# Performance work log

Measured on AMD Instinct MI355X. Metric: run time of the kernel, lower is better.

The kernel has to match this reference:

```python
import jax, jax.numpy as jnp
import numpy as np

N_NODES = 100000
N_EDGES = 600000
IN_FEATS = 128
N_HIDDEN = 128
N_CLASSES = 64


def _glorot(key, shape):
    fan_in, fan_out = shape[1], shape[0]
    lim = np.sqrt(6.0 / (fan_in + fan_out)).astype(np.float32)
    return jax.random.uniform(key, shape, jnp.float32, -lim, lim)


def setup_inputs() -> dict:
    key = jax.random.key(0)
    ks = jax.random.split(key, 12)
    x = jax.random.normal(ks[0], (N_NODES, IN_FEATS), jnp.float32)
    edge_src = jax.random.randint(ks[1], (N_EDGES,), 0, N_NODES, jnp.int64 if jax.config.jax_enable_x64 else jnp.int32)
    edge_dst = jax.random.randint(ks[2], (N_EDGES,), 0, N_NODES, jnp.int64 if jax.config.jax_enable_x64 else jnp.int32)
    dims = [(IN_FEATS, N_HIDDEN), (N_HIDDEN, N_HIDDEN), (N_HIDDEN, N_CLASSES)]
    inp = {"x": x, "edge_src": edge_src, "edge_dst": edge_dst}
    for i, (din, dout) in enumerate(dims, start=1):
        inp[f"W_self{i}"] = _glorot(ks[2 + 3 * i], (dout, din))
        inp[f"W_neigh{i}"] = _glorot(ks[3 + 3 * i], (dout, din))
        inp[f"b{i}"] = jnp.zeros((dout,), jnp.float32)
    return inp


def _sage_conv(h, edge_src, edge_dst, W_self, W_neigh, b):
    # mean-aggregate neighbor features: gather at src, segment-mean at dst
    msgs = h[edge_src]                                   # [E, din] irregular gather
    agg = jax.ops.segment_sum(msgs, edge_dst, num_segments=h.shape[0])
    deg = jax.ops.segment_sum(jnp.ones_like(edge_dst, dtype=h.dtype), edge_dst,
                              num_segments=h.shape[0])
    h_neigh = agg / jnp.maximum(deg, 1.0)[:, None]
    # fc_self(h) + fc_neigh(h_neigh) + bias  (DGL SAGEConv 'mean')
    return h @ W_self.T + h_neigh @ W_neigh.T + b


def reference(x, edge_src, edge_dst,
              W_self1, W_neigh1, b1,
              W_self2, W_neigh2, b2,
              W_self3, W_neigh3, b3):
    h = _sage_conv(x, edge_src, edge_dst, W_self1, W_neigh1, b1)
    h = jax.nn.relu(h)  # dropout is identity at inference
    h = _sage_conv(h, edge_src, edge_dst, W_self2, W_neigh2, b2)
    h = jax.nn.relu(h)
    h = _sage_conv(h, edge_src, edge_dst, W_self3, W_neigh3, b3)
    return h
```

## Files before the change

kernel.cpp:

```cpp
#include <hip/hip_runtime.h>

#define NN 100000
#define NE 600000
#define FD 128
#define NB ((NN + 255) / 256)

typedef __attribute__((ext_vector_type(8))) short bf16x8;
typedef __attribute__((ext_vector_type(4))) float f32x4;

__device__ __forceinline__ unsigned short f2bf(float x) {
    unsigned int u = __float_as_uint(x);
    u += 0x7FFFu + ((u >> 16) & 1u);
    return (unsigned short)(u >> 16);
}

__global__ __launch_bounds__(256) void hist_kernel(const int* __restrict__ dst,
                                                   int* __restrict__ cnt, int E) {
    int e = blockIdx.x * 256 + threadIdx.x;
    if (e < E) atomicAdd(&cnt[dst[e]], 1);
}

__global__ __launch_bounds__(256) void scan_blocks(const int* __restrict__ cnt,
                                                   int* __restrict__ bsum) {
    __shared__ int s[256];
    int i = blockIdx.x * 256 + threadIdx.x;
    int t = threadIdx.x;
    s[t] = (i < NN) ? cnt[i] : 0;
    __syncthreads();
    for (int off = 128; off > 0; off >>= 1) {
        if (t < off) s[t] += s[t + off];
        __syncthreads();
    }
    if (t == 0) bsum[blockIdx.x] = s[0];
}

__global__ __launch_bounds__(512) void scan_top(int* __restrict__ bsum,
                                                int* __restrict__ row_ptr) {
    __shared__ int s[512];
    int t = threadIdx.x;
    int v = (t < NB) ? bsum[t] : 0;
    s[t] = v;
    __syncthreads();
    for (int off = 1; off < 512; off <<= 1) {
        int x = (t >= off) ? s[t - off] : 0;
        __syncthreads();
        s[t] += x;
        __syncthreads();
    }
    if (t < NB) bsum[t] = s[t] - v;
    if (t == 0) row_ptr[NN] = NE;
}

__global__ __launch_bounds__(256) void scan_write(const int* __restrict__ cnt,
                                                  const int* __restrict__ bofs,
                                                  int* __restrict__ row_ptr) {
    __shared__ int s[256];
    int i = blockIdx.x * 256 + threadIdx.x;
    int t = threadIdx.x;
    int v = (i < NN) ? cnt[i] : 0;
    s[t] = v;
    __syncthreads();
    for (int off = 1; off < 256; off <<= 1) {
        int x = (t >= off) ? s[t - off] : 0;
        __syncthreads();
        s[t] += x;
        __syncthreads();
    }
    if (i < NN) row_ptr[i] = s[t] - v + bofs[blockIdx.x];
}

__global__ __launch_bounds__(256) void fill_kernel(const int* __restrict__ src,
                                                   const int* __restrict__ dst,
                                                   int* __restrict__ cursor,
                                                   int* __restrict__ col, int E) {
    int e = blockIdx.x * 256 + threadIdx.x;
    if (e < E) {
        int p = atomicAdd(&cursor[dst[e]], 1);
        col[p] = src[e];
    }
}

__global__ __launch_bounds__(256) void cvt_kernel(const float* __restrict__ x,
                                                  unsigned short* __restrict__ xb,
                                                  int n4) {
    int i = blockIdx.x * 256 + threadIdx.x;
    if (i < n4) {
        float4 v = reinterpret_cast<const float4*>(x)[i];
        uint2 o;
        o.x = (unsigned)f2bf(v.x) | ((unsigned)f2bf(v.y) << 16);
        o.y = (unsigned)f2bf(v.z) | ((unsigned)f2bf(v.w) << 16);
        reinterpret_cast<uint2*>(xb)[i] = o;
    }
}

__device__ __forceinline__ void bf2_acc(unsigned v, float& ax, float& ay) {
    ax += __uint_as_float(v << 16);
    ay += __uint_as_float(v & 0xFFFF0000u);
}

__global__ __launch_bounds__(256) void agg_kernel(const unsigned short* __restrict__ h,
                                                  const int* __restrict__ rp,
                                                  const int* __restrict__ col,
                                                  unsigned short* __restrict__ agg) {
    int w    = (blockIdx.x * 256 + threadIdx.x) >> 6;
    int lane = threadIdx.x & 63;
    if (w >= NN) return;
    int beg = __builtin_amdgcn_readfirstlane(rp[w]);
    int end = __builtin_amdgcn_readfirstlane(rp[w + 1]);
    const unsigned short* hl = h + lane * 2;
    float ax = 0.f, ay = 0.f;
    int e = beg;
    for (; e + 4 <= end; e += 4) {
        int s0 = col[e + 0], s1 = col[e + 1], s2 = col[e + 2], s3 = col[e + 3];
        unsigned v0 = *reinterpret_cast<const unsigned*>(hl + (size_t)s0 * FD);
        unsigned v1 = *reinterpret_cast<const unsigned*>(hl + (size_t)s1 * FD);
        unsigned v2 = *reinterpret_cast<const unsigned*>(hl + (size_t)s2 * FD);
        unsigned v3 = *reinterpret_cast<const unsigned*>(hl + (size_t)s3 * FD);
        bf2_acc(v0, ax, ay);
        bf2_acc(v1, ax, ay);
        bf2_acc(v2, ax, ay);
        bf2_acc(v3, ax, ay);
    }
    if (e + 2 <= end) {
        int s0 = col[e + 0], s1 = col[e + 1];
        unsigned v0 = *reinterpret_cast<const unsigned*>(hl + (size_t)s0 * FD);
        unsigned v1 = *reinterpret_cast<const unsigned*>(hl + (size_t)s1 * FD);
        bf2_acc(v0, ax, ay);
        bf2_acc(v1, ax, ay);
        e += 2;
    }
    if (e < end) {
        int s0 = col[e];
        unsigned v0 = *reinterpret_cast<const unsigned*>(hl + (size_t)s0 * FD);
        bf2_acc(v0, ax, ay);
    }
    float inv = 1.0f / fmaxf((float)(end - beg), 1.0f);
    ax *= inv;
    ay *= inv;
    *reinterpret_cast<unsigned*>(agg + (size_t)w * FD + lane * 2) =
        (unsigned)f2bf(ax) | ((unsigned)f2bf(ay) << 16);
}

template <int NCOLS, bool RELU, bool OUTBF16>
__global__ __launch_bounds__(256) void mfma_gemm(const unsigned short* __restrict__ Ah,
                                                 const unsigned short* __restrict__ Ag,
                                                 const float* __restrict__ Wself,
                                                 const float* __restrict__ Wneigh,
                                                 const float* __restrict__ bias,
                                                 void* __restrict__ outp, int N) {
    __shared__ char lds[65536];
    char* Al = lds;
    char* Bl = lds + 32768;

    const int t     = threadIdx.x;
    const int n0    = blockIdx.x * 64;
    const int jbase = blockIdx.y * 64;

#pragma unroll
    for (int p = 0; p < 8; ++p) {
        int c    = t + p * 256;
        int row  = c >> 5;
        int ch16 = c & 31;
        int k8   = ch16 * 8;
        int n    = n0 + row;
        uint4 v  = make_uint4(0u, 0u, 0u, 0u);
        if (n < N) {
            const unsigned short* src = (k8 < 128)
                ? Ah + (size_t)n * FD + k8
                : Ag + (size_t)n * FD + (k8 - 128);
            v = *reinterpret_cast<const uint4*>(src);
        }
        *reinterpret_cast<uint4*>(Al + ((row * 512 + ch16 * 16) ^ ((row & 7) << 4))) = v;
    }
#pragma unroll
    for (int p = 0; p < 8; ++p) {
        int c    = t + p * 256;
        int row  = c >> 5;
        int ch16 = c & 31;
        int k8   = ch16 * 8;
        int j    = jbase + row;
        const float* src = (k8 < 128) ? (Wself + (size_t)j * 128 + k8)
                                      : (Wneigh + (size_t)j * 128 + (k8 - 128));
        float4 f0 = *reinterpret_cast<const float4*>(src);
        float4 f1 = *reinterpret_cast<const float4*>(src + 4);
        uint4 pk;
        pk.x = (unsigned)f2bf(f0.x) | ((unsigned)f2bf(f0.y) << 16);
        pk.y = (unsigned)f2bf(f0.z) | ((unsigned)f2bf(f0.w) << 16);
        pk.z = (unsigned)f2bf(f1.x) | ((unsigned)f2bf(f1.y) << 16);
        pk.w = (unsigned)f2bf(f1.z) | ((unsigned)f2bf(f1.w) << 16);
        *reinterpret_cast<uint4*>(Bl + ((row * 512 + ch16 * 16) ^ ((row & 7) << 4))) = pk;
    }
    __syncthreads();

    const int w   = t >> 6;
    const int l   = t & 63;
    const int lo4 = l & 15;
    const int hi  = l >> 4;
    const int xr  = (lo4 & 7) << 4;

    f32x4 acc0 = {0.f, 0.f, 0.f, 0.f};
    f32x4 acc1 = {0.f, 0.f, 0.f, 0.f};
    f32x4 acc2 = {0.f, 0.f, 0.f, 0.f};
    f32x4 acc3 = {0.f, 0.f, 0.f, 0.f};

    const char* Arow = Al + (w * 16 + lo4) * 512;
#pragma unroll
    for (int ks = 0; ks < 8; ++ks) {
        int koff = (ks * 64 + hi * 16) ^ xr;
        bf16x8 a = *reinterpret_cast<const bf16x8*>(Arow + koff);
        bf16x8 b0 = *reinterpret_cast<const bf16x8*>(Bl + (0 * 16 + lo4) * 512 + koff);
        bf16x8 b1 = *reinterpret_cast<const bf16x8*>(Bl + (1 * 16 + lo4) * 512 + koff);
        bf16x8 b2 = *reinterpret_cast<const bf16x8*>(Bl + (2 * 16 + lo4) * 512 + koff);
        bf16x8 b3 = *reinterpret_cast<const bf16x8*>(Bl + (3 * 16 + lo4) * 512 + koff);
        acc0 = __builtin_amdgcn_mfma_f32_16x16x32_bf16(a, b0, acc0, 0, 0, 0);
        acc1 = __builtin_amdgcn_mfma_f32_16x16x32_bf16(a, b1, acc1, 0, 0, 0);
        acc2 = __builtin_amdgcn_mfma_f32_16x16x32_bf16(a, b2, acc2, 0, 0, 0);
        acc3 = __builtin_amdgcn_mfma_f32_16x16x32_bf16(a, b3, acc3, 0, 0, 0);
    }

    unsigned short* hout = (unsigned short*)outp;
    float* fout = (float*)outp;
    const int rbase = n0 + w * 16 + hi * 4;
#pragma unroll
    for (int f = 0; f < 4; ++f) {
        f32x4 acc = (f == 0) ? acc0 : (f == 1) ? acc1 : (f == 2) ? acc2 : acc3;
        int col = jbase + f * 16 + lo4;
        float bv = bias[col];
#pragma unroll
        for (int r = 0; r < 4; ++r) {
            int n = rbase + r;
            if (n < N) {
                float v = acc[r] + bv;
                if (RELU) v = fmaxf(v, 0.f);
                if (OUTBF16) hout[(size_t)n * 128 + col] = f2bf(v);
                else         fout[(size_t)n * NCOLS + col] = v;
            }
        }
    }
}

extern "C" void kernel_launch(void* const* d_in, const int* in_sizes, int n_in,
                              void* d_out, int out_size, void* d_ws, size_t ws_size,
                              hipStream_t stream) {
    const float* x        = (const float*)d_in[0];
    const int*   edge_src = (const int*)d_in[1];
    const int*   edge_dst = (const int*)d_in[2];
    const float* Ws1 = (const float*)d_in[3];
    const float* Wn1 = (const float*)d_in[4];
    const float* b1  = (const float*)d_in[5];
    const float* Ws2 = (const float*)d_in[6];
    const float* Wn2 = (const float*)d_in[7];
    const float* b2  = (const float*)d_in[8];
    const float* Ws3 = (const float*)d_in[9];
    const float* Wn3 = (const float*)d_in[10];
    const float* b3  = (const float*)d_in[11];
    float* out = (float*)d_out;

    unsigned short* x_bf = (unsigned short*)d_ws;
    unsigned short* h_a  = x_bf + (size_t)NN * FD;
    unsigned short* h_b  = h_a + (size_t)NN * FD;
    unsigned short* aggb = h_b + (size_t)NN * FD;
    int* cursor = (int*)(aggb + (size_t)NN * FD);
    int* bsum   = (int*)aggb;
    int* col_src = (int*)d_out;
    int* row_ptr = col_src + NE;

    const int edgeGrid = (NE + 255) / 256;
    const int aggGrid  = NN / 4;
    const int rowGrid  = (NN + 63) / 64;

    cvt_kernel<<<(NN * FD / 4 + 255) / 256, 256, 0, stream>>>(x, x_bf, NN * FD / 4);

    hipMemsetAsync(cursor, 0, (size_t)NN * sizeof(int), stream);
    hist_kernel<<<edgeGrid, 256, 0, stream>>>(edge_dst, cursor, NE);
    scan_blocks<<<NB, 256, 0, stream>>>(cursor, bsum);
    scan_top<<<1, 512, 0, stream>>>(bsum, row_ptr);
    scan_write<<<NB, 256, 0, stream>>>(cursor, bsum, row_ptr);
    hipMemcpyAsync(cursor, row_ptr, (size_t)NN * sizeof(int),
                   hipMemcpyDeviceToDevice, stream);
    fill_kernel<<<edgeGrid, 256, 0, stream>>>(edge_src, edge_dst, cursor,
                                              col_src, NE);

    agg_kernel<<<aggGrid, 256, 0, stream>>>(x_bf, row_ptr, col_src, aggb);
    mfma_gemm<128, true, true><<<dim3(rowGrid, 2), 256, 0, stream>>>(
        x_bf, aggb, Ws1, Wn1, b1, h_a, NN);

    agg_kernel<<<aggGrid, 256, 0, stream>>>(h_a, row_ptr, col_src, aggb);
    mfma_gemm<128, true, true><<<dim3(rowGrid, 2), 256, 0, stream>>>(
        h_a, aggb, Ws2, Wn2, b2, h_b, NN);

    agg_kernel<<<aggGrid, 256, 0, stream>>>(h_b, row_ptr, col_src, aggb);
    mfma_gemm<64, false, false><<<dim3(rowGrid, 1), 256, 0, stream>>>(
        h_b, aggb, Ws3, Wn3, b3, out, NN);
}
```

Baseline: 399.8 us.

## Pre-convert weights to bf16 once and cover all output columns per GEMM block

Adds a small kernel that converts each layer's self and neighbor weights to a packed bf16 buffer once, so GEMM blocks no longer reload and reconvert fp32 weights. Each GEMM block now computes the full output width instead of splitting columns over a second grid dimension, which halves how often the A tile is loaded. The K dimension is staged in two 128-wide chunks to cut LDS use, with an occupancy hint of 3 blocks. This adds extra syncs per block and places the weight buffers in spare output and cursor space, which relies on those regions being free at the time they are used.

After: 359.6 us. -10.0%, faster.

```diff
diff --git a/kernel.cpp b/kernel.cpp
--- a/kernel.cpp
+++ b/kernel.cpp
@@ -91,6 +91,23 @@
         o.y = (unsigned)f2bf(v.z) | ((unsigned)f2bf(v.w) << 16);
         reinterpret_cast<uint2*>(xb)[i] = o;
     }
+}
+
+__global__ __launch_bounds__(256) void wcvt_kernel(const float* __restrict__ Ws,
+                                                   const float* __restrict__ Wn,
+                                                   unsigned short* __restrict__ Wb,
+                                                   int rows) {
+    int tid = blockIdx.x * 256 + threadIdx.x;
+    if (tid >= rows * 64) return;
+    int row = tid >> 6;
+    int k   = (tid & 63) * 4;
+    const float* src = (k < 128) ? (Ws + (size_t)row * 128 + k)
+                                 : (Wn + (size_t)row * 128 + (k - 128));
+    float4 v = *reinterpret_cast<const float4*>(src);
+    uint2 o;
+    o.x = (unsigned)f2bf(v.x) | ((unsigned)f2bf(v.y) << 16);
+    o.y = (unsigned)f2bf(v.z) | ((unsigned)f2bf(v.w) << 16);
+    *reinterpret_cast<uint2*>(Wb + (size_t)row * 256 + k) = o;
 }
 
 __device__ __forceinline__ void bf2_acc(unsigned v, float& ax, float& ay) {
@@ -141,99 +158,80 @@
         (unsigned)f2bf(ax) | ((unsigned)f2bf(ay) << 16);
 }
 
-template <int NCOLS, bool RELU, bool OUTBF16>
-__global__ __launch_bounds__(256) void mfma_gemm(const unsigned short* __restrict__ Ah,
-                                                 const unsigned short* __restrict__ Ag,
-                                                 const float* __restrict__ Wself,
-                                                 const float* __restrict__ Wneigh,
-                                                 const float* __restrict__ bias,
-                                                 void* __restrict__ outp, int N) {
-    __shared__ char lds[65536];
+template <int BN, bool RELU, bool OUTBF16>
+__global__ __launch_bounds__(256, 3) void mfma_gemm(const unsigned short* __restrict__ Ah,
+                                                    const unsigned short* __restrict__ Ag,
+                                                    const unsigned short* __restrict__ Wb,
+                                                    const float* __restrict__ bias,
+                                                    void* __restrict__ outp, int N) {
+    __shared__ char lds[16384 + BN * 256];
     char* Al = lds;
-    char* Bl = lds + 32768;
-
-    const int t     = threadIdx.x;
-    const int n0    = blockIdx.x * 64;
-    const int jbase = blockIdx.y * 64;
-
-#pragma unroll
-    for (int p = 0; p < 8; ++p) {
-        int c    = t + p * 256;
-        int row  = c >> 5;
-        int ch16 = c & 31;
-        int k8   = ch16 * 8;
-        int n    = n0 + row;
-        uint4 v  = make_uint4(0u, 0u, 0u, 0u);
-        if (n < N) {
-            const unsigned short* src = (k8 < 128)
-                ? Ah + (size_t)n * FD + k8
-                : Ag + (size_t)n * FD + (k8 - 128);
-            v = *reinterpret_cast<const uint4*>(src);
-        }
-        *reinterpret_cast<uint4*>(Al + ((row * 512 + ch16 * 16) ^ ((row & 7) << 4))) = v;
-    }
-#pragma unroll
-    for (int p = 0; p < 8; ++p) {
-        int c    = t + p * 256;
-        int row  = c >> 5;
-        int ch16 = c & 31;
-        int k8   = ch16 * 8;
-        int j    = jbase + row;
-        const float* src = (k8 < 128) ? (Wself + (size_t)j * 128 + k8)
-                                      : (Wneigh + (size_t)j * 128 + (k8 - 128));
-        float4 f0 = *reinterpret_cast<const float4*>(src);
-        float4 f1 = *reinterpret_cast<const float4*>(src + 4);
-        uint4 pk;
-        pk.x = (unsigned)f2bf(f0.x) | ((unsigned)f2bf(f0.y) << 16);
-        pk.y = (unsigned)f2bf(f0.z) | ((unsigned)f2bf(f0.w) << 16);
-        pk.z = (unsigned)f2bf(f1.x) | ((unsigned)f2bf(f1.y) << 16);
-        pk.w = (unsigned)f2bf(f1.z) | ((unsigned)f2bf(f1.w) << 16);
-        *reinterpret_cast<uint4*>(Bl + ((row * 512 + ch16 * 16) ^ ((row & 7) << 4))) = pk;
-    }
-    __syncthreads();
-
+    char* Bl = lds + 16384;
+
+    const int t   = threadIdx.x;
+    const int n0  = blockIdx.x * 64;
     const int w   = t >> 6;
     const int l   = t & 63;
     const int lo4 = l & 15;
     const int hi  = l >> 4;
     const int xr  = (lo4 & 7) << 4;
 
-    f32x4 acc0 = {0.f, 0.f, 0.f, 0.f};
-    f32x4 acc1 = {0.f, 0.f, 0.f, 0.f};
-    f32x4 acc2 = {0.f, 0.f, 0.f, 0.f};
-    f32x4 acc3 = {0.f, 0.f, 0.f, 0.f};
-
-    const char* Arow = Al + (w * 16 + lo4) * 512;
-#pragma unroll
-    for (int ks = 0; ks < 8; ++ks) {
-        int koff = (ks * 64 + hi * 16) ^ xr;
-        bf16x8 a = *reinterpret_cast<const bf16x8*>(Arow + koff);
-        bf16x8 b0 = *reinterpret_cast<const bf16x8*>(Bl + (0 * 16 + lo4) * 512 + koff);
-        bf16x8 b1 = *reinterpret_cast<const bf16x8*>(Bl + (1 * 16 + lo4) * 512 + koff);
-        bf16x8 b2 = *reinterpret_cast<const bf16x8*>(Bl + (2 * 16 + lo4) * 512 + koff);
-        bf16x8 b3 = *reinterpret_cast<const bf16x8*>(Bl + (3 * 16 + lo4) * 512 + koff);
-        acc0 = __builtin_amdgcn_mfma_f32_16x16x32_bf16(a, b0, acc0, 0, 0, 0);
-        acc1 = __builtin_amdgcn_mfma_f32_16x16x32_bf16(a, b1, acc1, 0, 0, 0);
-        acc2 = __builtin_amdgcn_mfma_f32_16x16x32_bf16(a, b2, acc2, 0, 0, 0);
-        acc3 = __builtin_amdgcn_mfma_f32_16x16x32_bf16(a, b3, acc3, 0, 0, 0);
+    f32x4 acc[BN / 16];
+#pragma unroll
+    for (int f = 0; f < BN / 16; ++f) acc[f] = {0.f, 0.f, 0.f, 0.f};
+
+#pragma unroll
+    for (int kc = 0; kc < 2; ++kc) {
+        const unsigned short* Asrc = kc ? Ag : Ah;
+#pragma unroll
+        for (int p = 0; p < 4; ++p) {
+            int c   = t + p * 256;
+            int row = c >> 4;
+            int ch  = c & 15;
+            int n   = n0 + row;
+            uint4 v = make_uint4(0u, 0u, 0u, 0u);
+            if (n < N) v = *reinterpret_cast<const uint4*>(Asrc + (size_t)n * FD + ch * 8);
+            *reinterpret_cast<uint4*>(Al + ((row * 256 + ch * 16) ^ ((row & 7) << 4))) = v;
+        }
+#pragma unroll
+        for (int p = 0; p < BN / 16; ++p) {
+            int c   = t + p * 256;
+            int row = c >> 4;
+            int ch  = c & 15;
+            uint4 v = *reinterpret_cast<const uint4*>(Wb + (size_t)row * 256 + kc * 128 + ch * 8);
+            *reinterpret_cast<uint4*>(Bl + ((row * 256 + ch * 16) ^ ((row & 7) << 4))) = v;
+        }
+        __syncthreads();
+
+        const char* Arow = Al + (w * 16 + lo4) * 256;
+#pragma unroll
+        for (int ks = 0; ks < 4; ++ks) {
+            int koff = (ks * 64 + hi * 16) ^ xr;
+            bf16x8 a = *reinterpret_cast<const bf16x8*>(Arow + koff);
+#pragma unroll
+            for (int f = 0; f < BN / 16; ++f) {
+                bf16x8 b = *reinterpret_cast<const bf16x8*>(Bl + (f * 16 + lo4) * 256 + koff);
+                acc[f] = __builtin_amdgcn_mfma_f32_16x16x32_bf16(a, b, acc[f], 0, 0, 0);
+            }
+        }
+        __syncthreads();
     }
 
     unsigned short* hout = (unsigned short*)outp;
     float* fout = (float*)outp;
     const int rbase = n0 + w * 16 + hi * 4;
 #pragma unroll
-    for (int f = 0; f < 4; ++f) {
-        f32x4 acc = (f == 0) ? acc0 : (f == 1) ? acc1 : (f == 2) ? acc2 : acc3;
-        int col = jbase + f * 16 + lo4;
+    for (int f = 0; f < BN / 16; ++f) {
+        int col  = f * 16 + lo4;
         float bv = bias[col];
 #pragma unroll
         for (int r = 0; r < 4; ++r) {
             int n = rbase + r;
             if (n < N) {
-                float v = acc[r] + bv;
+                float v = acc[f][r] + bv;
                 if (RELU) v = fmaxf(v, 0.f);
                 if (OUTBF16) hout[(size_t)n * 128 + col] = f2bf(v);
-                else         fout[(size_t)n * NCOLS + col] = v;
+                else         fout[(size_t)n * BN + col] = v;
             }
         }
     }
@@ -264,12 +262,17 @@
     int* bsum   = (int*)aggb;
     int* col_src = (int*)d_out;
     int* row_ptr = col_src + NE;
+    unsigned short* wb1 = (unsigned short*)(col_src + NE + NN + 4);
+    unsigned short* wb2 = wb1 + 128 * 256;
+    unsigned short* wb3 = (unsigned short*)cursor;
 
     const int edgeGrid = (NE + 255) / 256;
     const int aggGrid  = NN / 4;
     const int rowGrid  = (NN + 63) / 64;
 
     cvt_kernel<<<(NN * FD / 4 + 255) / 256, 256, 0, stream>>>(x, x_bf, NN * FD / 4);
+    wcvt_kernel<<<32, 256, 0, stream>>>(Ws1, Wn1, wb1, 128);
+    wcvt_kernel<<<32, 256, 0, stream>>>(Ws2, Wn2, wb2, 128);
 
     hipMemsetAsync(cursor, 0, (size_t)NN * sizeof(int), stream);
     hist_kernel<<<edgeGrid, 256, 0, stream>>>(edge_dst, cursor, NE);
@@ -280,16 +283,17 @@
                    hipMemcpyDeviceToDevice, stream);
     fill_kernel<<<edgeGrid, 256, 0, stream>>>(edge_src, edge_dst, cursor,
                                               col_src, NE);
+    wcvt_kernel<<<16, 256, 0, stream>>>(Ws3, Wn3, wb3, 64);
 
     agg_kernel<<<aggGrid, 256, 0, stream>>>(x_bf, row_ptr, col_src, aggb);
-    mfma_gemm<128, true, true><<<dim3(rowGrid, 2), 256, 0, stream>>>(
-        x_bf, aggb, Ws1, Wn1, b1, h_a, NN);
+    mfma_gemm<128, true, true><<<rowGrid, 256, 0, stream>>>(
+        x_bf, aggb, wb1, b1, h_a, NN);
 
     agg_kernel<<<aggGrid, 256, 0, stream>>>(h_a, row_ptr, col_src, aggb);
-    mfma_gemm<128, true, true><<<dim3(rowGrid, 2), 256, 0, stream>>>(
-        h_a, aggb, Ws2, Wn2, b2, h_b, NN);
+    mfma_gemm<128, true, true><<<rowGrid, 256, 0, stream>>>(
+        h_a, aggb, wb2, b2, h_b, NN);
 
     agg_kernel<<<aggGrid, 256, 0, stream>>>(h_b, row_ptr, col_src, aggb);
-    mfma_gemm<64, false, false><<<dim3(rowGrid, 1), 256, 0, stream>>>(
-        h_b, aggb, Ws3, Wn3, b3, out, NN);
-}
+    mfma_gemm<64, false, false><<<rowGrid, 256, 0, stream>>>(
+        h_b, aggb, wb3, b3, out, NN);
+}
```
